# Kernel tuning notes

Measured on AMD Instinct MI355X. Metric: run time of the kernel, lower is better.

## Reference

```python
import math
import jax, jax.numpy as jnp
import numpy as np

NUM_HEADS = 16
QUERY_SIZE = 1024
SEQ = 2048
HEAD = QUERY_SIZE // NUM_HEADS  # qk_size = vo_size = 64


def setup_inputs() -> dict:
    key = jax.random.key(0)
    ks = jax.random.split(key, 8)
    s = 0.02
    query = jax.random.normal(ks[0], (SEQ, QUERY_SIZE), jnp.float32)
    key_ = jax.random.normal(ks[1], (SEQ, QUERY_SIZE), jnp.float32)
    value = jax.random.normal(ks[2], (SEQ, QUERY_SIZE), jnp.float32)
    # causal mask (mask='causal' with state=None -> offset 0)
    mask = jnp.tril(jnp.ones((SEQ, SEQ), dtype=bool))
    Wq = jax.random.normal(ks[3], (QUERY_SIZE, QUERY_SIZE), jnp.float32) * s
    Wk = jax.random.normal(ks[4], (QUERY_SIZE, QUERY_SIZE), jnp.float32) * s
    Wv = jax.random.normal(ks[5], (QUERY_SIZE, QUERY_SIZE), jnp.float32) * s
    Wo = jax.random.normal(ks[6], (QUERY_SIZE, QUERY_SIZE), jnp.float32) * s
    return {"query": query, "key_": key_, "value": value, "mask": mask,
            "Wq": Wq, "Wk": Wk, "Wv": Wv, "Wo": Wo}


def reference(query, key_, value, mask, Wq, Wk, Wv, Wo):
    H, D = NUMS = NUM_HEADS, HEAD
    S = query.shape[0]
    inv_sqrt_d = 1.0 / math.sqrt(D)
    # per-token linear projections, split into heads: [S, H, D]
    q = (query @ Wq.T).reshape(S, H, D)
    k = (key_ @ Wk.T).reshape(S, H, D)
    v = (value @ Wv.T).reshape(S, H, D)
    # NOTE: original divides BOTH q and k by sqrt(d) (effective 1/d scaling)
    q = q * inv_sqrt_d
    k = k * inv_sqrt_d
    # logits per head: [H, S, S]
    logits = jnp.einsum('shd,Shd->hsS', q, k)
    logits = jnp.where(mask[None, :, :], logits, jnp.finfo(logits.dtype).min)
    # per-head GLOBAL max subtraction, softmax in fp32, cast back (faithful)
    m = jnp.max(logits, axis=(1, 2), keepdims=True)
    weights = jax.nn.softmax((logits - m).astype(jnp.float32), axis=-1).astype(query.dtype)
    attn = jnp.einsum('hsS,ShD->shD', weights, v).reshape(S, H * D)
    return attn @ Wo.T
```

## Files before the change

### kernel.cpp

```cpp
#include <hip/hip_runtime.h>
#include <hip/hip_bf16.h>

typedef __bf16 bf16_t;
typedef __bf16 bf16x8 __attribute__((ext_vector_type(8)));
typedef float f32x4 __attribute__((ext_vector_type(4)));

#define MFMA(A, B, C) __builtin_amdgcn_mfma_f32_16x16x32_bf16(A, B, C, 0, 0, 0)

__global__ __launch_bounds__(256) void cvt_all(
    const float* __restrict__ q, const float* __restrict__ k, const float* __restrict__ v,
    const float* __restrict__ wq, const float* __restrict__ wk,
    const float* __restrict__ wv, const float* __restrict__ wo,
    bf16_t* __restrict__ xq, bf16_t* __restrict__ xk, bf16_t* __restrict__ xv,
    bf16_t* __restrict__ ywq, bf16_t* __restrict__ ywk,
    bf16_t* __restrict__ ywv, bf16_t* __restrict__ ywo)
{
  const long gid = (long)blockIdx.x * 256 + threadIdx.x;
  const float* s; bf16_t* d; long off; float sc = 1.0f;
  if (gid < 262144)       { s = q;  d = xq;  off = gid; }
  else if (gid < 524288)  { s = k;  d = xk;  off = gid - 262144; }
  else if (gid < 786432)  { s = v;  d = xv;  off = gid - 524288; }
  else if (gid < 917504)  { s = wq; d = ywq; off = gid - 786432;  sc = 0.125f; }
  else if (gid < 1048576) { s = wk; d = ywk; off = gid - 917504;  sc = 0.125f; }
  else if (gid < 1179648) { s = wv; d = ywv; off = gid - 1048576; }
  else                    { s = wo; d = ywo; off = gid - 1179648; }
  const float* p = s + off * 8;
  float4 a = *(const float4*)p, b = *(const float4*)(p + 4);
  bf16x8 o;
  o[0] = (bf16_t)(a.x * sc); o[1] = (bf16_t)(a.y * sc);
  o[2] = (bf16_t)(a.z * sc); o[3] = (bf16_t)(a.w * sc);
  o[4] = (bf16_t)(b.x * sc); o[5] = (bf16_t)(b.y * sc);
  o[6] = (bf16_t)(b.z * sc); o[7] = (bf16_t)(b.w * sc);
  *(bf16x8*)(d + off * 8) = o;
}

__device__ __forceinline__ void gemm_core(const bf16_t* __restrict__ A,
                                          const bf16_t* __restrict__ W,
                                          int bm, int bn,
                                          bf16_t* As, bf16_t* Bs,
                                          f32x4 (&acc)[4][2])
{
  const int tid = threadIdx.x, lane = tid & 63, wave = tid >> 6;
  const int l15 = lane & 15, l4 = lane >> 4;
  const int wm = (wave >> 1) * 64, wn = (wave & 1) * 32;

  bf16x8 ra[4], rb[2];
#pragma unroll
  for (int i = 0; i < 4; ++i) {
    int id = tid + 256 * i, row = id >> 3, c = id & 7;
    ra[i] = *(const bf16x8*)(A + (size_t)(bm + row) * 1024 + c * 8);
  }
#pragma unroll
  for (int i = 0; i < 2; ++i) {
    int id = tid + 256 * i, row = id >> 3, c = id & 7;
    rb[i] = *(const bf16x8*)(W + (size_t)(bn + row) * 1024 + c * 8);
  }

#pragma unroll
  for (int s = 0; s < 16; ++s) {
    __syncthreads();
#pragma unroll
    for (int i = 0; i < 4; ++i) {
      int id = tid + 256 * i, row = id >> 3, c = id & 7;
      *(bf16x8*)(&As[row * 64 + 8 * (c ^ (row & 7))]) = ra[i];
    }
#pragma unroll
    for (int i = 0; i < 2; ++i) {
      int id = tid + 256 * i, row = id >> 3, c = id & 7;
      *(bf16x8*)(&Bs[row * 64 + 8 * (c ^ (row & 7))]) = rb[i];
    }
    __syncthreads();
    if (s + 1 < 16) {
      const int k0 = (s + 1) * 64;
#pragma unroll
      for (int i = 0; i < 4; ++i) {
        int id = tid + 256 * i, row = id >> 3, c = id & 7;
        ra[i] = *(const bf16x8*)(A + (size_t)(bm + row) * 1024 + k0 + c * 8);
      }
#pragma unroll
      for (int i = 0; i < 2; ++i) {
        int id = tid + 256 * i, row = id >> 3, c = id & 7;
        rb[i] = *(const bf16x8*)(W + (size_t)(bn + row) * 1024 + k0 + c * 8);
      }
    }
#pragma unroll
    for (int ks = 0; ks < 2; ++ks) {
      bf16x8 af[4], bfr[2];
#pragma unroll
      for (int i = 0; i < 4; ++i)
        af[i] = *(const bf16x8*)(&As[(wm + i * 16 + l15) * 64 + 8 * ((ks * 4 + l4) ^ (l15 & 7))]);
#pragma unroll
      for (int j = 0; j < 2; ++j)
        bfr[j] = *(const bf16x8*)(&Bs[(wn + j * 16 + l15) * 64 + 8 * ((ks * 4 + l4) ^ (l15 & 7))]);
#pragma unroll
      for (int i = 0; i < 4; ++i)
#pragma unroll
        for (int j = 0; j < 2; ++j)
          acc[i][j] = MFMA(af[i], bfr[j], acc[i][j]);
    }
  }
}

__global__ __launch_bounds__(256) void gemm_qkv(
    const bf16_t* __restrict__ xq, const bf16_t* __restrict__ xk, const bf16_t* __restrict__ xv,
    const bf16_t* __restrict__ ywq, const bf16_t* __restrict__ ywk, const bf16_t* __restrict__ ywv,
    bf16_t* __restrict__ qo, bf16_t* __restrict__ ko, bf16_t* __restrict__ vt)
{
  __shared__ __align__(16) bf16_t As[128 * 64];
  __shared__ __align__(16) bf16_t Bs[64 * 64];
  const int z = blockIdx.z;
  const bf16_t* A = z == 0 ? xq : z == 1 ? xk : xv;
  const bf16_t* W = z == 0 ? ywq : z == 1 ? ywk : ywv;
  const int bm = blockIdx.x * 128, bn = blockIdx.y * 64;
  f32x4 acc[4][2] = {};
  gemm_core(A, W, bm, bn, As, Bs, acc);
  const int tid = threadIdx.x, lane = tid & 63, wave = tid >> 6;
  const int l15 = lane & 15, l4 = lane >> 4;
  const int wm = (wave >> 1) * 64, wn = (wave & 1) * 32;
  if (z < 2) {
    bf16_t* C = z == 0 ? qo : ko;
#pragma unroll
    for (int i = 0; i < 4; ++i)
#pragma unroll
      for (int j = 0; j < 2; ++j)
#pragma unroll
        for (int r = 0; r < 4; ++r)
          C[(size_t)(bm + wm + i * 16 + 4 * l4 + r) * 1024 + bn + wn + j * 16 + l15] =
              (bf16_t)acc[i][j][r];
  } else {
#pragma unroll
    for (int i = 0; i < 4; ++i)
#pragma unroll
      for (int j = 0; j < 2; ++j)
#pragma unroll
        for (int r = 0; r < 4; ++r)
          vt[(size_t)(bn + wn + j * 16 + l15) * 2048 + bm + wm + i * 16 + 4 * l4 + r] =
              (bf16_t)acc[i][j][r];
  }
}

__global__ __launch_bounds__(256) void gemm_out(
    const bf16_t* __restrict__ ctx, const bf16_t* __restrict__ ywo, float* __restrict__ out)
{
  __shared__ __align__(16) bf16_t As[128 * 64];
  __shared__ __align__(16) bf16_t Bs[64 * 64];
  const int bm = blockIdx.x * 128, bn = blockIdx.y * 64;
  f32x4 acc[4][2] = {};
  gemm_core(ctx, ywo, bm, bn, As, Bs, acc);
  const int tid = threadIdx.x, lane = tid & 63, wave = tid >> 6;
  const int l15 = lane & 15, l4 = lane >> 4;
  const int wm = (wave >> 1) * 64, wn = (wave & 1) * 32;
#pragma unroll
  for (int i = 0; i < 4; ++i)
#pragma unroll
    for (int j = 0; j < 2; ++j)
#pragma unroll
      for (int r = 0; r < 4; ++r)
        out[(size_t)(bm + wm + i * 16 + 4 * l4 + r) * 1024 + bn + wn + j * 16 + l15] =
            acc[i][j][r];
}

__global__ __launch_bounds__(512) void attn512(
    const bf16_t* __restrict__ Qb, const bf16_t* __restrict__ Kb,
    const bf16_t* __restrict__ Vt, bf16_t* __restrict__ Ctx)
{
  __shared__ __align__(16) bf16_t Ks[2][128 * 64];
  __shared__ __align__(16) bf16_t Vs[2][64 * 128];
  __shared__ __align__(16) bf16_t Ps[8][16 * 64];

  const int bid = blockIdx.x;
  const int h = 2 * (bid & 7) + ((bid >> 3) >> 4);
  const int jp = (bid >> 3) & 15;
  const int hoff = h * 64;
  const int tid = threadIdx.x;
  const int lane = tid & 63, wave = tid >> 6;
  const int g = wave & 3, kh = wave >> 2;
  const int l15 = lane & 15, l4 = lane >> 4;
  const int l7 = l15 & 7;

  const int qtA = jp, qtB = 31 - jp;
  const int qbA = qtA * 64, qbB = qtB * 64;
  const int nscA = qtA / 2 + 1, nscB = qtB / 2 + 1;

  const int qrA = qbA + g * 16 + l15, qrB = qbB + g * 16 + l15;
  bf16x8 qA0 = *(const bf16x8*)(Qb + (size_t)qrA * 1024 + hoff + 8 * l4);
  bf16x8 qA1 = *(const bf16x8*)(Qb + (size_t)qrA * 1024 + hoff + 32 + 8 * l4);
  bf16x8 qB0 = *(const bf16x8*)(Qb + (size_t)qrB * 1024 + hoff + 8 * l4);
  bf16x8 qB1 = *(const bf16x8*)(Qb + (size_t)qrB * 1024 + hoff + 32 + 8 * l4);

  f32x4 oA[4] = {}, oB[4] = {};
  float dA[4] = {0.f, 0.f, 0.f, 0.f}, dB[4] = {0.f, 0.f, 0.f, 0.f};

  bf16x8 rk[2], rv[2];
  auto issue = [&](int sc) {
    const int t0 = sc * 128;
#pragma unroll
    for (int i = 0; i < 2; ++i) {
      const int id = tid + 512 * i;
      const int kr = id >> 3, kc = id & 7;
      rk[i] = *(const bf16x8*)(Kb + (size_t)(t0 + kr) * 1024 + hoff + 8 * kc);
      const int vr = id >> 4, vc = id & 15;
      rv[i] = *(const bf16x8*)(Vt + (size_t)(hoff + vr) * 2048 + t0 + 8 * vc);
    }
  };
  auto commit = [&](int buf) {
#pragma unroll
    for (int i = 0; i < 2; ++i) {
      const int id = tid + 512 * i;
      const int kr = id >> 3, kc = id & 7;
      *(bf16x8*)(&Ks[buf][kr * 64 + 8 * (kc ^ (kr & 7))]) = rk[i];
      const int vr = id >> 4, vc = id & 15;
      *(bf16x8*)(&Vs[buf][vr * 128 + 8 * (vc ^ (vr & 7))]) = rv[i];
    }
  };

  auto process = [&](int sc, int cur, int qb, const bf16x8& q0, const bf16x8& q1,
                     f32x4 (&oacc)[4], float (&den)[4]) {
    if (128 * sc + 64 * kh > qb + g * 16 + 15) return;
    const int tb = 128 * sc + 64 * kh;
#pragma unroll
    for (int sub = 0; sub < 4; ++sub) {
      const int krow = 64 * kh + 16 * sub + l15;
      bf16x8 kf0 = *(const bf16x8*)(&Ks[cur][krow * 64 + 8 * (l4 ^ l7)]);
      bf16x8 kf1 = *(const bf16x8*)(&Ks[cur][krow * 64 + 8 * ((4 + l4) ^ l7)]);
      f32x4 sv = {};
      sv = MFMA(q0, kf0, sv);
      sv = MFMA(q1, kf1, sv);
      const int t = tb + 16 * sub + l15;
#pragma unroll
      for (int r = 0; r < 4; ++r) {
        const int qq = qb + g * 16 + 4 * l4 + r;
        const float p = (t <= qq) ? __expf(sv[r]) : 0.0f;
        const bf16_t pb = (bf16_t)p;
        den[r] += (float)pb;
        const int prow = 4 * l4 + r;
        const int pch = 2 * sub + (l15 >> 3);
        Ps[wave][prow * 64 + 8 * (pch ^ (prow & 7)) + l7] = pb;
      }
    }
    asm volatile("s_waitcnt lgkmcnt(0)" ::: "memory");
#pragma unroll
    for (int ks = 0; ks < 2; ++ks) {
      bf16x8 pf = *(const bf16x8*)(&Ps[wave][l15 * 64 + 8 * ((ks * 4 + l4) ^ l7)]);
#pragma unroll
      for (int db = 0; db < 4; ++db) {
        bf16x8 vf = *(const bf16x8*)(&Vs[cur][(db * 16 + l15) * 128 + 64 * kh + 8 * ((ks * 4 + l4) ^ l7)]);
        oacc[db] = MFMA(pf, vf, oacc[db]);
      }
    }
  };

  issue(0);
  commit(0);
  int cur = 0;
  for (int sc = 0; sc < nscB; ++sc) {
    const bool pre = (sc + 1 < nscB);
    if (pre) issue(sc + 1);
    __syncthreads();
    process(sc, cur, qbB, qB0, qB1, oB, dB);
    if (sc < nscA) process(sc, cur, qbA, qA0, qA1, oA, dA);
    if (pre) commit(cur ^ 1);
    cur ^= 1;
  }

  __syncthreads();
#pragma unroll
  for (int r = 0; r < 4; ++r)
#pragma unroll
    for (int m = 1; m < 16; m <<= 1) {
      dA[r] += __shfl_xor(dA[r], m, 64);
      dB[r] += __shfl_xor(dB[r], m, 64);
    }
  float* Os = (float*)(&Ks[0][0]);
  float* Ds = (float*)(&Vs[0][0]);
  if (kh == 1) {
#pragma unroll
    for (int r = 0; r < 4; ++r) {
      const int row = g * 16 + 4 * l4 + r;
#pragma unroll
      for (int db = 0; db < 4; ++db) {
        Os[(0 * 64 + row) * 64 + db * 16 + l15] = oA[db][r];
        Os[(1 * 64 + row) * 64 + db * 16 + l15] = oB[db][r];
      }
      if (l15 == 0) { Ds[0 * 64 + row] = dA[r]; Ds[1 * 64 + row] = dB[r]; }
    }
  }
  __syncthreads();
  if (kh == 0) {
#pragma unroll
    for (int r = 0; r < 4; ++r) {
      const int row = g * 16 + 4 * l4 + r;
      const float iA = 1.0f / (dA[r] + Ds[0 * 64 + row]);
      const float iB = 1.0f / (dB[r] + Ds[1 * 64 + row]);
#pragma unroll
      for (int db = 0; db < 4; ++db) {
        const float vA = oA[db][r] + Os[(0 * 64 + row) * 64 + db * 16 + l15];
        const float vB = oB[db][r] + Os[(1 * 64 + row) * 64 + db * 16 + l15];
        Ctx[(size_t)(qbA + row) * 1024 + hoff + db * 16 + l15] = (bf16_t)(vA * iA);
        Ctx[(size_t)(qbB + row) * 1024 + hoff + db * 16 + l15] = (bf16_t)(vB * iB);
      }
    }
  }
}

extern "C" void kernel_launch(void* const* d_in, const int* in_sizes, int n_in,
                              void* d_out, int out_size, void* d_ws, size_t ws_size,
                              hipStream_t stream)
{
  const float* query = (const float*)d_in[0];
  const float* key_  = (const float*)d_in[1];
  const float* value = (const float*)d_in[2];
  const float* Wq = (const float*)d_in[4];
  const float* Wk = (const float*)d_in[5];
  const float* Wv = (const float*)d_in[6];
  const float* Wo = (const float*)d_in[7];
  float* out = (float*)d_out;

  const size_t SE = (size_t)2048 * 1024, EE = (size_t)1024 * 1024;
  bf16_t* xq  = (bf16_t*)d_ws;
  bf16_t* xk  = xq + SE;
  bf16_t* xv  = xk + SE;
  bf16_t* wq  = xv + SE;
  bf16_t* wk  = wq + EE;
  bf16_t* wv  = wk + EE;
  bf16_t* wo  = wv + EE;
  bf16_t* qo  = wo + EE;
  bf16_t* ko  = qo + SE;
  bf16_t* vt  = ko + SE;
  bf16_t* ctx = vt + SE;

  cvt_all<<<5120, 256, 0, stream>>>(query, key_, value, Wq, Wk, Wv, Wo,
                                    xq, xk, xv, wq, wk, wv, wo);
  gemm_qkv<<<dim3(16, 16, 3), 256, 0, stream>>>(xq, xk, xv, wq, wk, wv, qo, ko, vt);
  attn512<<<256, 512, 0, stream>>>(qo, ko, vt, ctx);
  gemm_out<<<dim3(16, 16), 256, 0, stream>>>(ctx, wo, out);
}
```

Before: 73.54 us.

## Double-buffer GEMM tiles with direct global-to-LDS async loads

Replaces the register-staged global load plus LDS store in the shared GEMM core with global_load_lds direct copies into a double-buffered LDS tile. The XOR swizzle moves to the global address side so the LDS layout is unchanged. The goal is to cut VGPR staging and LDS store instructions and to overlap the next tile's fetch with MFMA work. LDS use doubles to 48KB per block, which may reduce occupancy, and correctness depends on the wait/barrier semantics of the async loads.

New measurement: 72.08 us. -2.0%, faster.

```diff
diff --git a/kernel.cpp b/kernel.cpp
--- a/kernel.cpp
+++ b/kernel.cpp
@@ -6,6 +6,10 @@
 typedef float f32x4 __attribute__((ext_vector_type(4)));
 
 #define MFMA(A, B, C) __builtin_amdgcn_mfma_f32_16x16x32_bf16(A, B, C, 0, 0, 0)
+
+#define GLL16(g, l) __builtin_amdgcn_global_load_lds(                      \
+    (const __attribute__((address_space(1))) void*)(g),                    \
+    (__attribute__((address_space(3))) void*)(l), 16, 0, 0)
 
 __global__ __launch_bounds__(256) void cvt_all(
     const float* __restrict__ q, const float* __restrict__ k, const float* __restrict__ v,
@@ -37,67 +41,54 @@
 __device__ __forceinline__ void gemm_core(const bf16_t* __restrict__ A,
                                           const bf16_t* __restrict__ W,
                                           int bm, int bn,
-                                          bf16_t* As, bf16_t* Bs,
+                                          bf16_t (&As)[2][128 * 64],
+                                          bf16_t (&Bs)[2][64 * 64],
                                           f32x4 (&acc)[4][2])
 {
   const int tid = threadIdx.x, lane = tid & 63, wave = tid >> 6;
-  const int l15 = lane & 15, l4 = lane >> 4;
+  const int l15 = lane & 15, l4 = lane >> 4, l7 = l15 & 7;
   const int wm = (wave >> 1) * 64, wn = (wave & 1) * 32;
 
-  bf16x8 ra[4], rb[2];
-#pragma unroll
-  for (int i = 0; i < 4; ++i) {
-    int id = tid + 256 * i, row = id >> 3, c = id & 7;
-    ra[i] = *(const bf16x8*)(A + (size_t)(bm + row) * 1024 + c * 8);
-  }
-#pragma unroll
-  for (int i = 0; i < 2; ++i) {
-    int id = tid + 256 * i, row = id >> 3, c = id & 7;
-    rb[i] = *(const bf16x8*)(W + (size_t)(bn + row) * 1024 + c * 8);
-  }
-
+  auto stage = [&](int buf, int k0) {
+#pragma unroll
+    for (int i = 0; i < 4; ++i) {
+      const int id = i * 256 + tid;
+      const int row = id >> 3, cph = id & 7;
+      GLL16(A + (size_t)(bm + row) * 1024 + k0 + 8 * (cph ^ (row & 7)),
+            &As[buf][(i * 256 + wave * 64) * 8]);
+    }
+#pragma unroll
+    for (int i = 0; i < 2; ++i) {
+      const int id = i * 256 + tid;
+      const int row = id >> 3, cph = id & 7;
+      GLL16(W + (size_t)(bn + row) * 1024 + k0 + 8 * (cph ^ (row & 7)),
+            &Bs[buf][(i * 256 + wave * 64) * 8]);
+    }
+  };
+
+  stage(0, 0);
 #pragma unroll
   for (int s = 0; s < 16; ++s) {
+    if (s + 1 < 16) stage((s + 1) & 1, (s + 1) * 64);
     __syncthreads();
-#pragma unroll
-    for (int i = 0; i < 4; ++i) {
-      int id = tid + 256 * i, row = id >> 3, c = id & 7;
-      *(bf16x8*)(&As[row * 64 + 8 * (c ^ (row & 7))]) = ra[i];
-    }
-#pragma unroll
-    for (int i = 0; i < 2; ++i) {
-      int id = tid + 256 * i, row = id >> 3, c = id & 7;
-      *(bf16x8*)(&Bs[row * 64 + 8 * (c ^ (row & 7))]) = rb[i];
-    }
-    __syncthreads();
-    if (s + 1 < 16) {
-      const int k0 = (s + 1) * 64;
-#pragma unroll
-      for (int i = 0; i < 4; ++i) {
-        int id = tid + 256 * i, row = id >> 3, c = id & 7;
-        ra[i] = *(const bf16x8*)(A + (size_t)(bm + row) * 1024 + k0 + c * 8);
-      }
-#pragma unroll
-      for (int i = 0; i < 2; ++i) {
-        int id = tid + 256 * i, row = id >> 3, c = id & 7;
-        rb[i] = *(const bf16x8*)(W + (size_t)(bn + row) * 1024 + k0 + c * 8);
-      }
-    }
+    const bf16_t* as = As[s & 1];
+    const bf16_t* bs = Bs[s & 1];
 #pragma unroll
     for (int ks = 0; ks < 2; ++ks) {
       bf16x8 af[4], bfr[2];
 #pragma unroll
       for (int i = 0; i < 4; ++i)
-        af[i] = *(const bf16x8*)(&As[(wm + i * 16 + l15) * 64 + 8 * ((ks * 4 + l4) ^ (l15 & 7))]);
+        af[i] = *(const bf16x8*)(&as[(wm + i * 16 + l15) * 64 + 8 * ((ks * 4 + l4) ^ l7)]);
 #pragma unroll
       for (int j = 0; j < 2; ++j)
-        bfr[j] = *(const bf16x8*)(&Bs[(wn + j * 16 + l15) * 64 + 8 * ((ks * 4 + l4) ^ (l15 & 7))]);
+        bfr[j] = *(const bf16x8*)(&bs[(wn + j * 16 + l15) * 64 + 8 * ((ks * 4 + l4) ^ l7)]);
 #pragma unroll
       for (int i = 0; i < 4; ++i)
 #pragma unroll
         for (int j = 0; j < 2; ++j)
           acc[i][j] = MFMA(af[i], bfr[j], acc[i][j]);
     }
+    __syncthreads();
   }
 }
 
@@ -106,8 +97,8 @@
     const bf16_t* __restrict__ ywq, const bf16_t* __restrict__ ywk, const bf16_t* __restrict__ ywv,
     bf16_t* __restrict__ qo, bf16_t* __restrict__ ko, bf16_t* __restrict__ vt)
 {
-  __shared__ __align__(16) bf16_t As[128 * 64];
-  __shared__ __align__(16) bf16_t Bs[64 * 64];
+  __shared__ __align__(16) bf16_t As[2][128 * 64];
+  __shared__ __align__(16) bf16_t Bs[2][64 * 64];
   const int z = blockIdx.z;
   const bf16_t* A = z == 0 ? xq : z == 1 ? xk : xv;
   const bf16_t* W = z == 0 ? ywq : z == 1 ? ywk : ywv;
@@ -142,8 +133,8 @@
 __global__ __launch_bounds__(256) void gemm_out(
     const bf16_t* __restrict__ ctx, const bf16_t* __restrict__ ywo, float* __restrict__ out)
 {
-  __shared__ __align__(16) bf16_t As[128 * 64];
-  __shared__ __align__(16) bf16_t Bs[64 * 64];
+  __shared__ __align__(16) bf16_t As[2][128 * 64];
+  __shared__ __align__(16) bf16_t Bs[2][64 * 64];
   const int bm = blockIdx.x * 128, bn = blockIdx.y * 64;
   f32x4 acc[4][2] = {};
   gemm_core(ctx, ywo, bm, bn, As, Bs, acc);
```
